# Optimization experiments

Measured on AMD Instinct MI355X. Metric: run time of the kernel, lower is better.

## Reference

```python
import jax, jax.numpy as jnp
import numpy as np

NQ = 7
D = 2 ** NQ              # 128
B = 1024
T = D * (D + 1) // 2     # 8256
DS = 0.25                # downscaling

_rows, _cols = np.tril_indices(D)
ROWS = jnp.asarray(_rows)
COLS = jnp.asarray(_cols)

_s = np.float32(1.0 / np.sqrt(2.0))
_H = np.array([[_s, _s], [_s, -_s]], dtype=np.complex64)          # Hadamard (X basis)
_Sdag = np.array([[1, 0], [0, -1j]], dtype=np.complex64)
GATES = jnp.asarray(np.stack([_H, _H @ _Sdag, np.eye(2)]).astype(np.complex64))  # [X, Y, Z] rotations, (3,2,2)


def _loss(flat, t, state_ri, tgt, basis):
    # Reconstruct real symmetric matrix from lower-triangular flatten: (B, D, D)
    M = (jnp.zeros((B, D, D), flat.dtype)
         .at[:, ROWS, COLS].set(flat)
         .at[:, COLS, ROWS].set(flat))
    # U = expm(-1j*DS*t*M); M is real symmetric so use eigh (exact, batched)
    w, V = jnp.linalg.eigh(M)                      # w:(B,D) V:(B,D,D)
    ang = DS * t[:, None] * w                      # (B, D)
    phase = (jnp.cos(ang) - 1j * jnp.sin(ang)).astype(jnp.complex64)
    Vc = V.astype(jnp.complex64)
    U = jnp.einsum('bik,bk,bjk->bij', Vc, phase, Vc)
    # Evolve initial state: U rho U^dagger
    rho0 = (state_ri[..., 0] + 1j * state_ri[..., 1]).astype(jnp.complex64)
    ev = U @ rho0 @ U.conj().swapaxes(-1, -2)
    # Per-sample Kronecker rotation: kron of per-qubit 2x2 gates (batched)
    rot = GATES[basis]                             # (B, NQ, 2, 2)
    full = rot[:, 0]
    for q in range(1, NQ):
        d = full.shape[-1]
        full = jnp.einsum('bij,bkl->bikjl', full, rot[:, q]).reshape(B, d * 2, d * 2)
    rr = full @ ev @ full.conj().swapaxes(-1, -2)
    # Measurement probabilities and NLL
    diag = jnp.diagonal(rr, axis1=-2, axis2=-1)    # (B, D)
    probs = jnp.abs(diag) ** 2
    probs = probs / probs.sum(axis=1, keepdims=True)
    tp = jnp.take_along_axis(probs, tgt[:, None], axis=1)[:, 0]
    tp = jnp.clip(tp, 1e-12, None)
    return -jnp.mean(jnp.log(tp)) / NQ


def setup_inputs() -> dict:
    key = jax.random.key(0)
    k1, k2, k3, k4, k5 = jax.random.split(key, 5)
    return {
        'predictor_flat': jax.random.normal(k1, (B, T), dtype=jnp.float32),
        'time': jax.random.uniform(k2, (B,), dtype=jnp.float32),
        'input_state': jax.random.normal(k3, (B, D, D, 2), dtype=jnp.float32),
        'target_indices': jax.random.randint(k4, (B,), 0, D),
        'basis_indices': jax.random.randint(k5, (B, NQ), 0, 3),
    }


def reference(predictor_flat, time, input_state, target_indices, basis_indices):
    return _loss(predictor_flat, time, input_state, target_indices, basis_indices)
```

## Files before the change

### kernel.cpp

```cpp
#include <hip/hip_runtime.h>
#include <math.h>

#define DD    128
#define NQQ   7
#define NB    1024
#define TRI   8256
#define NSQ   2
#define CSTR  136
#define FSTR  132

typedef short  bf16x8 __attribute__((ext_vector_type(8)));
typedef short  s16x4  __attribute__((ext_vector_type(4)));
typedef float  f32x16 __attribute__((ext_vector_type(16)));

__device__ __forceinline__ void split2(float v, unsigned short& h, unsigned short& l) {
  unsigned u = __builtin_bit_cast(unsigned, v);
  float hf = __builtin_bit_cast(float, u & 0xFFFF0000u);
  float lf = v - hf;
  h = (unsigned short)(u >> 16);
  l = (unsigned short)(__builtin_bit_cast(unsigned, lf) >> 16);
}
__device__ __forceinline__ float bf2f(unsigned short s) {
  return __builtin_bit_cast(float, ((unsigned)s) << 16);
}
__device__ __forceinline__ f32x16 MF(bf16x8 a, bf16x8 b, f32x16 c) {
  return __builtin_amdgcn_mfma_f32_32x32x16_bf16(a, b, c, 0, 0, 0);
}
__device__ __forceinline__ bf16x8 NEG(bf16x8 a) {
  int4 u = __builtin_bit_cast(int4, a);
  u.x ^= 0x80008000; u.y ^= 0x80008000; u.z ^= 0x80008000; u.w ^= 0x80008000;
  return __builtin_bit_cast(bf16x8, u);
}
__device__ __forceinline__ bf16x8 LDF(const unsigned short* C, int row, int s, int hb) {
  return *reinterpret_cast<const bf16x8*>(C + row * CSTR + s * 16 + hb * 8);
}

__global__ __launch_bounds__(512) __attribute__((amdgpu_waves_per_eu(2, 2)))
void loss_k(
    const float* __restrict__ flat,
    const float* __restrict__ timev,
    const float* __restrict__ state,
    const int*   __restrict__ tgt,
    const int*   __restrict__ basis,
    float* __restrict__ ws)
{
  __shared__ __align__(16) char lds[4 * 128 * CSTR * 2 + 8192];
  unsigned short* C0 = (unsigned short*)lds;
  unsigned short* C1 = C0 + 128 * CSTR;
  unsigned short* C2 = C1 + 128 * CSTR;
  unsigned short* C3 = C2 + 128 * CSTR;
  float* AUX = (float*)(lds + 4 * 128 * CSTR * 2);
  float* Urf = (float*)lds;
  float* Uif = Urf + 128 * FSTR;

  const int b    = blockIdx.x;
  const int tid  = threadIdx.x;
  const int wid  = tid >> 6;
  const int lane = tid & 63;
  const int l31  = lane & 31;
  const int hb   = lane >> 5;

  const int tr    = wid >> 1;
  const int tcb   = (wid & 1) * 2;
  const int arow  = 32 * tr + l31;
  const int bcol0 = 32 * tcb + l31;
  const int bcol1 = 32 * (tcb + 1) + l31;

  const float tval  = timev[b];
  const float alpha = 0.25f * tval * 0.25f;
  const float* fb = flat + (size_t)b * TRI;

#define STORE_TILE(PREG, SCALE, BCOL, DH, DL) do {                         \
    _Pragma("unroll")                                                      \
    for (int q_ = 0; q_ < 4; ++q_) {                                       \
      s16x4 hh_, ll_;                                                      \
      _Pragma("unroll")                                                    \
      for (int rr_ = 0; rr_ < 4; ++rr_) {                                  \
        unsigned short h_, l_;                                             \
        split2((SCALE) * (PREG)[4 * q_ + rr_], h_, l_);                    \
        hh_[rr_] = (short)h_; ll_[rr_] = (short)l_;                        \
      }                                                                    \
      int off_ = (BCOL) * CSTR + 32 * tr + 8 * q_ + 4 * hb;                \
      *(s16x4*)((DH) + off_) = hh_; *(s16x4*)((DL) + off_) = ll_;          \
    }                                                                      \
  } while (0)

  for (int e = tid; e < DD * DD; e += 512) {
    int i = e >> 7, j = e & 127;
    int r = i >= j ? i : j, c = i >= j ? j : i;
    float v = alpha * fb[(r * (r + 1)) / 2 + c];
    unsigned short h, l; split2(v, h, l);
    C0[i * CSTR + j] = h;  C1[i * CSTR + j] = l;
  }
  __syncthreads();

  f32x16 p0, p1, Cc0, Cc1, Qc0, Qc1;

#pragma unroll
  for (int e = 0; e < 16; ++e) { p0[e] = 0.0f; p1[e] = 0.0f; }
#pragma unroll
  for (int s = 0; s < 8; ++s) {
    bf16x8 ah = LDF(C0, arow, s, hb),  al = LDF(C1, arow, s, hb);
    bf16x8 b0h = LDF(C0, bcol0, s, hb), b0l = LDF(C1, bcol0, s, hb);
    bf16x8 b1h = LDF(C0, bcol1, s, hb), b1l = LDF(C1, bcol1, s, hb);
    p0 = MF(ah, b0h, p0); p0 = MF(ah, b0l, p0); p0 = MF(al, b0h, p0);
    p1 = MF(ah, b1h, p1); p1 = MF(ah, b1l, p1); p1 = MF(al, b1h, p1);
  }
  __syncthreads();
#pragma unroll
  for (int q = 0; q < 4; ++q) {
#pragma unroll
    for (int rr = 0; rr < 4; ++rr) {
      int e = 4 * q + rr;
      int rg = 32 * tr + 8 * q + 4 * hb + rr;
      float i0 = (rg == bcol0) ? 1.0f : 0.0f;
      float i1 = (rg == bcol1) ? 1.0f : 0.0f;
      Cc0[e] = i0 - 0.5f * p0[e];            Cc1[e] = i1 - 0.5f * p1[e];
      Qc0[e] = i0 - 0.16666667f * p0[e];     Qc1[e] = i1 - 0.16666667f * p1[e];
    }
  }
  STORE_TILE(p0, 1.0f, bcol0, C2, C3);
  STORE_TILE(p1, 1.0f, bcol1, C2, C3);
  __syncthreads();

#pragma unroll
  for (int e = 0; e < 16; ++e) { p0[e] = 0.0f; p1[e] = 0.0f; }
#pragma unroll
  for (int s = 0; s < 8; ++s) {
    bf16x8 ah = LDF(C2, arow, s, hb),  al = LDF(C3, arow, s, hb);
    bf16x8 b0h = LDF(C2, bcol0, s, hb), b0l = LDF(C3, bcol0, s, hb);
    bf16x8 b1h = LDF(C2, bcol1, s, hb), b1l = LDF(C3, bcol1, s, hb);
    p0 = MF(ah, b0h, p0); p0 = MF(ah, b0l, p0); p0 = MF(al, b0h, p0);
    p1 = MF(ah, b1h, p1); p1 = MF(ah, b1l, p1); p1 = MF(al, b1h, p1);
  }
  __syncthreads();
#pragma unroll
  for (int e = 0; e < 16; ++e) {
    Cc0[e] += 4.1666668e-2f * p0[e];  Cc1[e] += 4.1666668e-2f * p1[e];
    Qc0[e] += 8.3333333e-3f * p0[e];  Qc1[e] += 8.3333333e-3f * p1[e];
  }
  STORE_TILE(p0, 1.0f, bcol0, C0, C1);
  STORE_TILE(p1, 1.0f, bcol1, C0, C1);
  __syncthreads();

  const float CJ[9] = {0.f, 0.f, 0.f, -1.3888889e-3f, 2.4801587e-5f,
                       -2.7557319e-7f, 2.0876757e-9f, -1.1470746e-11f, 4.7794773e-14f};
  const float QJ[8] = {0.f, 0.f, 0.f, -1.9841270e-4f, 2.7557319e-6f,
                       -2.5052108e-8f, 1.6059044e-10f, -7.6471637e-13f};
#pragma unroll
  for (int j = 3; j <= 8; ++j) {
#pragma unroll
    for (int e = 0; e < 16; ++e) { p0[e] = 0.0f; p1[e] = 0.0f; }
#pragma unroll
    for (int s = 0; s < 8; ++s) {
      bf16x8 ah = LDF(C2, arow, s, hb),  al = LDF(C3, arow, s, hb);
      bf16x8 b0h = LDF(C0, bcol0, s, hb), b0l = LDF(C1, bcol0, s, hb);
      bf16x8 b1h = LDF(C0, bcol1, s, hb), b1l = LDF(C1, bcol1, s, hb);
      p0 = MF(ah, b0h, p0); p0 = MF(ah, b0l, p0); p0 = MF(al, b0h, p0);
      p1 = MF(ah, b1h, p1); p1 = MF(ah, b1l, p1); p1 = MF(al, b1h, p1);
    }
    __syncthreads();
#pragma unroll
    for (int e = 0; e < 16; ++e) { Cc0[e] += CJ[j] * p0[e]; Cc1[e] += CJ[j] * p1[e]; }
    if (j < 8) {
#pragma unroll
      for (int e = 0; e < 16; ++e) { Qc0[e] += QJ[j] * p0[e]; Qc1[e] += QJ[j] * p1[e]; }
      STORE_TILE(p0, 1.0f, bcol0, C0, C1);
      STORE_TILE(p1, 1.0f, bcol1, C0, C1);
    }
    __syncthreads();
  }

  STORE_TILE(Qc0, 1.0f, bcol0, C2, C3);
  STORE_TILE(Qc1, 1.0f, bcol1, C2, C3);
  for (int e = tid; e < DD * DD; e += 512) {
    int i = e >> 7, j = e & 127;
    int r = i >= j ? i : j, c = i >= j ? j : i;
    float v = alpha * fb[(r * (r + 1)) / 2 + c];
    unsigned short h, l; split2(v, h, l);
    C0[i * CSTR + j] = h;  C1[i * CSTR + j] = l;
  }
  __syncthreads();

#pragma unroll
  for (int e = 0; e < 16; ++e) { p0[e] = 0.0f; p1[e] = 0.0f; }
#pragma unroll
  for (int s = 0; s < 8; ++s) {
    bf16x8 ah = LDF(C0, arow, s, hb),  al = LDF(C1, arow, s, hb);
    bf16x8 b0h = LDF(C2, bcol0, s, hb), b0l = LDF(C3, bcol0, s, hb);
    bf16x8 b1h = LDF(C2, bcol1, s, hb), b1l = LDF(C3, bcol1, s, hb);
    p0 = MF(ah, b0h, p0); p0 = MF(ah, b0l, p0); p0 = MF(al, b0h, p0);
    p1 = MF(ah, b1h, p1); p1 = MF(ah, b1l, p1); p1 = MF(al, b1h, p1);
  }
  __syncthreads();

  STORE_TILE(Cc0, 1.0f, bcol0, C0, C1);
  STORE_TILE(Cc1, 1.0f, bcol1, C0, C1);
  STORE_TILE(p0, -1.0f, bcol0, C2, C3);
  STORE_TILE(p1, -1.0f, bcol1, C2, C3);
  __syncthreads();

  for (int sq = 0; sq < NSQ; ++sq) {
    f32x16 cr0, ci0, cr1, ci1;
#pragma unroll
    for (int e = 0; e < 16; ++e) { cr0[e] = 0; ci0[e] = 0; cr1[e] = 0; ci1[e] = 0; }
#pragma unroll
    for (int s = 0; s < 8; ++s) {
      bf16x8 aRh = LDF(C0, arow, s, hb), aRl = LDF(C1, arow, s, hb);
      bf16x8 aIh = LDF(C2, arow, s, hb), aIl = LDF(C3, arow, s, hb);
      bf16x8 aIhN = NEG(aIh), aIlN = NEG(aIl);
      bf16x8 bRh0 = LDF(C0, bcol0, s, hb), bRl0 = LDF(C1, bcol0, s, hb);
      bf16x8 bIh0 = LDF(C2, bcol0, s, hb), bIl0 = LDF(C3, bcol0, s, hb);
      bf16x8 bRh1 = LDF(C0, bcol1, s, hb), bRl1 = LDF(C1, bcol1, s, hb);
      bf16x8 bIh1 = LDF(C2, bcol1, s, hb), bIl1 = LDF(C3, bcol1, s, hb);
      cr0 = MF(aRh, bRh0, cr0); cr0 = MF(aRh, bRl0, cr0); cr0 = MF(aRl, bRh0, cr0);
      cr0 = MF(aIhN, bIh0, cr0); cr0 = MF(aIhN, bIl0, cr0); cr0 = MF(aIlN, bIh0, cr0);
      ci0 = MF(aRh, bIh0, ci0); ci0 = MF(aRh, bIl0, ci0); ci0 = MF(aRl, bIh0, ci0);
      cr1 = MF(aRh, bRh1, cr1); cr1 = MF(aRh, bRl1, cr1); cr1 = MF(aRl, bRh1, cr1);
      cr1 = MF(aIhN, bIh1, cr1); cr1 = MF(aIhN, bIl1, cr1); cr1 = MF(aIlN, bIh1, cr1);
      ci1 = MF(aRh, bIh1, ci1); ci1 = MF(aRh, bIl1, ci1); ci1 = MF(aRl, bIh1, ci1);
    }
    __syncthreads();
    if (sq < NSQ - 1) {
      STORE_TILE(cr0, 1.0f, bcol0, C0, C1);
      STORE_TILE(ci0, 2.0f, bcol0, C2, C3);
      STORE_TILE(cr1, 1.0f, bcol1, C0, C1);
      STORE_TILE(ci1, 2.0f, bcol1, C2, C3);
    } else {
#pragma unroll
      for (int q = 0; q < 4; ++q) {
        int off0 = bcol0 * FSTR + 32 * tr + 8 * q + 4 * hb;
        int off1 = bcol1 * FSTR + 32 * tr + 8 * q + 4 * hb;
        *(float4*)(Urf + off0) = make_float4(cr0[4*q], cr0[4*q+1], cr0[4*q+2], cr0[4*q+3]);
        *(float4*)(Uif + off0) = make_float4(2.0f*ci0[4*q], 2.0f*ci0[4*q+1], 2.0f*ci0[4*q+2], 2.0f*ci0[4*q+3]);
        *(float4*)(Urf + off1) = make_float4(cr1[4*q], cr1[4*q+1], cr1[4*q+2], cr1[4*q+3]);
        *(float4*)(Uif + off1) = make_float4(2.0f*ci1[4*q], 2.0f*ci1[4*q+1], 2.0f*ci1[4*q+2], 2.0f*ci1[4*q+3]);
      }
    }
    __syncthreads();
  }

  const int* bq = basis + b * NQQ;
  const float sv = 0.70710678118654752f;
  for (int q = 0; q < NQQ; ++q) {
    int g = bq[q];
    if (g == 2) continue;
    const int bit = 6 - q;
    float g00r, g01r, g01i, g10r, g11r, g11i;
    if (g == 0) { g00r = sv; g01r = sv; g01i = 0;   g10r = sv; g11r = -sv; g11i = 0;  }
    else        { g00r = sv; g01r = 0;  g01i = -sv; g10r = sv; g11r = 0;   g11i = sv; }
    for (int jj = tid; jj < 64 * 32; jj += 512) {
      int cg = jj & 31;
      int p  = jj >> 5;
      int low = p & ((1 << bit) - 1);
      int i0 = ((p >> bit) << (bit + 1)) | low;
      int i1 = i0 | (1 << bit);
      float4 a0 = *(float4*)(Urf + i0 * FSTR + 4 * cg);
      float4 b0 = *(float4*)(Uif + i0 * FSTR + 4 * cg);
      float4 a1 = *(float4*)(Urf + i1 * FSTR + 4 * cg);
      float4 b1 = *(float4*)(Uif + i1 * FSTR + 4 * cg);
      float4 n0r, n0i, n1r, n1i;
#define BFLY(cc) { \
      float A0 = a0.cc, B0 = b0.cc, A1 = a1.cc, B1 = b1.cc; \
      n0r.cc = g00r * A0 + g01r * A1 - g01i * B1; \
      n0i.cc = g00r * B0 + g01r * B1 + g01i * A1; \
      n1r.cc = g10r * A0 + g11r * A1 - g11i * B1; \
      n1i.cc = g10r * B0 + g11r * B1 + g11i * A1; }
      BFLY(x) BFLY(y) BFLY(z) BFLY(w)
#undef BFLY
      *(float4*)(Urf + i0 * FSTR + 4 * cg) = n0r;
      *(float4*)(Uif + i0 * FSTR + 4 * cg) = n0i;
      *(float4*)(Urf + i1 * FSTR + 4 * cg) = n1r;
      *(float4*)(Uif + i1 * FSTR + 4 * cg) = n1i;
    }
    __syncthreads();
  }

  {
    const int i  = tid >> 2;
    const int j0 = (tid & 3) * 32;
    float vr[32], vi[32];
#pragma unroll
    for (int c = 0; c < 8; ++c) {
      float4 x = *(float4*)(Urf + i * FSTR + j0 + 4 * c);
      vr[4*c+0] = x.x; vr[4*c+1] = x.y; vr[4*c+2] = x.z; vr[4*c+3] = x.w;
      float4 y = *(float4*)(Uif + i * FSTR + j0 + 4 * c);
      vi[4*c+0] = y.x; vi[4*c+1] = y.y; vi[4*c+2] = y.z; vi[4*c+3] = y.w;
    }
    __syncthreads();
#pragma unroll
    for (int blkc = 0; blkc < 4; ++blkc) {
      bf16x8 h, lo, h2, lo2;
#pragma unroll
      for (int e2 = 0; e2 < 8; ++e2) {
        unsigned short hh, ll;
        split2(vr[blkc * 8 + e2], hh, ll);  h[e2] = (short)hh;  lo[e2] = (short)ll;
        split2(vi[blkc * 8 + e2], hh, ll);  h2[e2] = (short)hh; lo2[e2] = (short)ll;
      }
      int off = i * CSTR + j0 + blkc * 8;
      *(bf16x8*)(C0 + off) = h;  *(bf16x8*)(C1 + off) = lo;
      *(bf16x8*)(C2 + off) = h2; *(bf16x8*)(C3 + off) = lo2;
    }
    __syncthreads();
  }

  const int slab = wid >> 1;
  const int part = wid & 1;
  const float* srow = state + (size_t)b * (DD * DD * 2) + (size_t)(32 * slab + l31) * 256;

#pragma unroll 1
  for (int ch = 0; ch < 2; ++ch) {
    const int n40 = 2 * ch;
    const int n41 = 2 * ch + 1;
    f32x16 w0, w1;
#pragma unroll
    for (int e = 0; e < 16; ++e) { w0[e] = 0; w1[e] = 0; }

    for (int s = 0; s < 8; ++s) {
      const float* pp = srow + (s * 16 + hb * 8) * 2;
      float4 q0 = *(const float4*)(pp);
      float4 q1 = *(const float4*)(pp + 4);
      float4 q2 = *(const float4*)(pp + 8);
      float4 q3 = *(const float4*)(pp + 12);
      float re[8] = {q0.x, q0.z, q1.x, q1.z, q2.x, q2.z, q3.x, q3.z};
      float im[8] = {q0.y, q0.w, q1.y, q1.w, q2.y, q2.w, q3.y, q3.w};
      bf16x8 rh, rl, ihh, ill;
#pragma unroll
      for (int e2 = 0; e2 < 8; ++e2) {
        unsigned short hh, ll;
        split2(re[e2], hh, ll); rh[e2] = (short)hh;  rl[e2] = (short)ll;
        split2(im[e2], hh, ll); ihh[e2] = (short)hh; ill[e2] = (short)ll;
      }
      bf16x8 rhn = NEG(rh), rln = NEG(rl);
#define P4N4(WREG, N4) do {                                                \
    int gcol_ = 32 * (N4) + l31;                                           \
    bf16x8 gRh = LDF(C0, gcol_, s, hb), gRl = LDF(C1, gcol_, s, hb);       \
    bf16x8 gIh = LDF(C2, gcol_, s, hb), gIl = LDF(C3, gcol_, s, hb);       \
    if (part == 0) {                                                       \
      WREG = MF(rh, gRh, WREG);  WREG = MF(rh, gRl, WREG);  WREG = MF(rl, gRh, WREG); \
      WREG = MF(ihh, gIh, WREG); WREG = MF(ihh, gIl, WREG); WREG = MF(ill, gIh, WREG); \
    } else {                                                               \
      WREG = MF(ihh, gRh, WREG); WREG = MF(ihh, gRl, WREG); WREG = MF(ill, gRh, WREG); \
      WREG = MF(rhn, gIh, WREG); WREG = MF(rhn, gIl, WREG); WREG = MF(rln, gIh, WREG); \
    }                                                                      \
  } while (0)
      P4N4(w0, n40); P4N4(w1, n41);
#undef P4N4
    }

#define P4DOT(WREG, N4) do {                                               \
    int gcol_ = 32 * (N4) + l31;                                           \
    float a1 = 0.0f, a2 = 0.0f;                                            \
    _Pragma("unroll")                                                      \
    for (int q_ = 0; q_ < 4; ++q_) {                                       \
      int koff = 32 * slab + 8 * q_ + 4 * hb;                              \
      s16x4 grh = *(const s16x4*)(C0 + gcol_ * CSTR + koff);               \
      s16x4 grl = *(const s16x4*)(C1 + gcol_ * CSTR + koff);               \
      s16x4 gih = *(const s16x4*)(C2 + gcol_ * CSTR + koff);               \
      s16x4 gil = *(const s16x4*)(C3 + gcol_ * CSTR + koff);               \
      _Pragma("unroll")                                                    \
      for (int rr_ = 0; rr_ < 4; ++rr_) {                                  \
        float wv = WREG[4 * q_ + rr_];                                     \
        float gr = bf2f((unsigned short)grh[rr_]) + bf2f((unsigned short)grl[rr_]); \
        float gi = bf2f((unsigned short)gih[rr_]) + bf2f((unsigned short)gil[rr_]); \
        a1 = fmaf(gr, wv, a1); a2 = fmaf(gi, wv, a2);                      \
      }                                                                    \
    }                                                                      \
    a1 += __shfl_xor(a1, 32); a2 += __shfl_xor(a2, 32);                    \
    if (lane < 32) {                                                       \
      AUX[((part * 2 + 0) * 4 + slab) * 128 + 32 * (N4) + l31] = a1;       \
      AUX[((part * 2 + 1) * 4 + slab) * 128 + 32 * (N4) + l31] = a2;       \
    }                                                                      \
  } while (0)
    P4DOT(w0, n40); P4DOT(w1, n41);
#undef P4DOT
  }
  __syncthreads();

  if (tid < 128) {
    float s0 = 0, s1 = 0, s2 = 0, s3 = 0;
#pragma unroll
    for (int sl = 0; sl < 4; ++sl) {
      s0 += AUX[(0 * 4 + sl) * 128 + tid];
      s1 += AUX[(1 * 4 + sl) * 128 + tid];
      s2 += AUX[(2 * 4 + sl) * 128 + tid];
      s3 += AUX[(3 * 4 + sl) * 128 + tid];
    }
    float dr = s0 - s3, di = s2 + s1;
    AUX[tid] = dr * dr + di * di;
  }
  __syncthreads();
  if (tid < 64) {
    float ps = AUX[tid] + AUX[tid + 64];
#pragma unroll
    for (int o = 32; o >= 1; o >>= 1) ps += __shfl_xor(ps, o);
    if (tid == 0) {
      float pt = AUX[tgt[b]];
      float tp = fmaxf(pt / ps, 1e-12f);
      ws[b] = -logf(tp) * (1.0f / (float)NQQ);
    }
  }
#undef STORE_TILE
}

__global__ __launch_bounds__(256) void reduce_k(const float* __restrict__ ws,
                                                float* __restrict__ out)
{
  __shared__ float s[256];
  const int tid = threadIdx.x;
  float v = ws[tid] + ws[tid + 256] + ws[tid + 512] + ws[tid + 768];
  s[tid] = v;
  __syncthreads();
  for (int o = 128; o > 0; o >>= 1) {
    if (tid < o) s[tid] += s[tid + o];
    __syncthreads();
  }
  if (tid == 0) out[0] = s[0] * (1.0f / (float)NB);
}

extern "C" void kernel_launch(void* const* d_in, const int* in_sizes, int n_in,
                              void* d_out, int out_size, void* d_ws, size_t ws_size,
                              hipStream_t stream) {
  const float* flat  = (const float*)d_in[0];
  const float* tv    = (const float*)d_in[1];
  const float* st    = (const float*)d_in[2];
  const int*   tgt   = (const int*)d_in[3];
  const int*   basis = (const int*)d_in[4];
  float* out = (float*)d_out;
  float* ws  = (float*)d_ws;

  hipLaunchKernelGGL(loss_k, dim3(NB), dim3(512), 0, stream,
                     flat, tv, st, tgt, basis, ws);
  hipLaunchKernelGGL(reduce_k, dim3(1), dim3(256), 0, stream, ws, out);
}
```

Baseline: 523.0 us.

## Double block to 1024 threads with one output tile per wave and bf16-split butterflies

Grows the block from 512 to 1024 threads, so each of the 16 waves computes a single 32x32 MFMA tile instead of two, and the final state-product loop runs as one pass with the work spread across more waves. The Kronecker butterfly stage now operates directly on the split bf16 hi/lo LDS buffers instead of a separate fp32 copy of U. This removes the fp32 staging pass and its conversion back to bf16. In exchange, register budget per thread drops, the waves_per_eu hint is removed, and every butterfly pass pays extra split and recombine arithmetic.

Result: slower. 935.9 us (+78.9%).

```diff
diff --git a/kernel.cpp b/kernel.cpp
--- a/kernel.cpp
+++ b/kernel.cpp
@@ -5,9 +5,7 @@
 #define NQQ   7
 #define NB    1024
 #define TRI   8256
-#define NSQ   2
 #define CSTR  136
-#define FSTR  132
 
 typedef short  bf16x8 __attribute__((ext_vector_type(8)));
 typedef short  s16x4  __attribute__((ext_vector_type(4)));
@@ -35,8 +33,7 @@
   return *reinterpret_cast<const bf16x8*>(C + row * CSTR + s * 16 + hb * 8);
 }
 
-__global__ __launch_bounds__(512) __attribute__((amdgpu_waves_per_eu(2, 2)))
-void loss_k(
+__global__ __launch_bounds__(1024) void loss_k(
     const float* __restrict__ flat,
     const float* __restrict__ timev,
     const float* __restrict__ state,
@@ -50,8 +47,6 @@
   unsigned short* C2 = C1 + 128 * CSTR;
   unsigned short* C3 = C2 + 128 * CSTR;
   float* AUX = (float*)(lds + 4 * 128 * CSTR * 2);
-  float* Urf = (float*)lds;
-  float* Uif = Urf + 128 * FSTR;
 
   const int b    = blockIdx.x;
   const int tid  = threadIdx.x;
@@ -60,17 +55,16 @@
   const int l31  = lane & 31;
   const int hb   = lane >> 5;
 
-  const int tr    = wid >> 1;
-  const int tcb   = (wid & 1) * 2;
-  const int arow  = 32 * tr + l31;
-  const int bcol0 = 32 * tcb + l31;
-  const int bcol1 = 32 * (tcb + 1) + l31;
+  const int tr   = wid >> 2;
+  const int tc   = wid & 3;
+  const int arow = 32 * tr + l31;
+  const int bcol = 32 * tc + l31;
 
   const float tval  = timev[b];
   const float alpha = 0.25f * tval * 0.25f;
   const float* fb = flat + (size_t)b * TRI;
 
-#define STORE_TILE(PREG, SCALE, BCOL, DH, DL) do {                         \
+#define STORE_TILE(PREG, SCALE, DH, DL) do {                               \
     _Pragma("unroll")                                                      \
     for (int q_ = 0; q_ < 4; ++q_) {                                       \
       s16x4 hh_, ll_;                                                      \
@@ -80,12 +74,23 @@
         split2((SCALE) * (PREG)[4 * q_ + rr_], h_, l_);                    \
         hh_[rr_] = (short)h_; ll_[rr_] = (short)l_;                        \
       }                                                                    \
-      int off_ = (BCOL) * CSTR + 32 * tr + 8 * q_ + 4 * hb;                \
+      int off_ = bcol * CSTR + 32 * tr + 8 * q_ + 4 * hb;                  \
       *(s16x4*)((DH) + off_) = hh_; *(s16x4*)((DL) + off_) = ll_;          \
     }                                                                      \
   } while (0)
 
-  for (int e = tid; e < DD * DD; e += 512) {
+#define PROD(AH, AL, BH, BL) do {                                          \
+    _Pragma("unroll")                                                      \
+    for (int e_ = 0; e_ < 16; ++e_) p[e_] = 0.0f;                          \
+    _Pragma("unroll")                                                      \
+    for (int s_ = 0; s_ < 8; ++s_) {                                       \
+      bf16x8 ah_ = LDF(AH, arow, s_, hb), al_ = LDF(AL, arow, s_, hb);     \
+      bf16x8 bh_ = LDF(BH, bcol, s_, hb), bl_ = LDF(BL, bcol, s_, hb);     \
+      p = MF(ah_, bh_, p); p = MF(ah_, bl_, p); p = MF(al_, bh_, p);       \
+    }                                                                      \
+  } while (0)
+
+  for (int e = tid; e < DD * DD; e += 1024) {
     int i = e >> 7, j = e & 127;
     int r = i >= j ? i : j, c = i >= j ? j : i;
     float v = alpha * fb[(r * (r + 1)) / 2 + c];
@@ -94,86 +99,56 @@
   }
   __syncthreads();
 
-  f32x16 p0, p1, Cc0, Cc1, Qc0, Qc1;
-
-#pragma unroll
-  for (int e = 0; e < 16; ++e) { p0[e] = 0.0f; p1[e] = 0.0f; }
-#pragma unroll
-  for (int s = 0; s < 8; ++s) {
-    bf16x8 ah = LDF(C0, arow, s, hb),  al = LDF(C1, arow, s, hb);
-    bf16x8 b0h = LDF(C0, bcol0, s, hb), b0l = LDF(C1, bcol0, s, hb);
-    bf16x8 b1h = LDF(C0, bcol1, s, hb), b1l = LDF(C1, bcol1, s, hb);
-    p0 = MF(ah, b0h, p0); p0 = MF(ah, b0l, p0); p0 = MF(al, b0h, p0);
-    p1 = MF(ah, b1h, p1); p1 = MF(ah, b1l, p1); p1 = MF(al, b1h, p1);
-  }
+  f32x16 p, Cc, Qc;
+
+  PROD(C0, C1, C0, C1);
   __syncthreads();
 #pragma unroll
   for (int q = 0; q < 4; ++q) {
 #pragma unroll
     for (int rr = 0; rr < 4; ++rr) {
       int e = 4 * q + rr;
-      int rg = 32 * tr + 8 * q + 4 * hb + rr;
-      float i0 = (rg == bcol0) ? 1.0f : 0.0f;
-      float i1 = (rg == bcol1) ? 1.0f : 0.0f;
-      Cc0[e] = i0 - 0.5f * p0[e];            Cc1[e] = i1 - 0.5f * p1[e];
-      Qc0[e] = i0 - 0.16666667f * p0[e];     Qc1[e] = i1 - 0.16666667f * p1[e];
-    }
-  }
-  STORE_TILE(p0, 1.0f, bcol0, C2, C3);
-  STORE_TILE(p1, 1.0f, bcol1, C2, C3);
-  __syncthreads();
-
-#pragma unroll
-  for (int e = 0; e < 16; ++e) { p0[e] = 0.0f; p1[e] = 0.0f; }
-#pragma unroll
-  for (int s = 0; s < 8; ++s) {
-    bf16x8 ah = LDF(C2, arow, s, hb),  al = LDF(C3, arow, s, hb);
-    bf16x8 b0h = LDF(C2, bcol0, s, hb), b0l = LDF(C3, bcol0, s, hb);
-    bf16x8 b1h = LDF(C2, bcol1, s, hb), b1l = LDF(C3, bcol1, s, hb);
-    p0 = MF(ah, b0h, p0); p0 = MF(ah, b0l, p0); p0 = MF(al, b0h, p0);
-    p1 = MF(ah, b1h, p1); p1 = MF(ah, b1l, p1); p1 = MF(al, b1h, p1);
-  }
+      float i0 = ((32 * tr + 8 * q + 4 * hb + rr) == bcol) ? 1.0f : 0.0f;
+      Cc[e] = i0 - 0.5f * p[e];
+      Qc[e] = i0 - 0.16666667f * p[e];
+    }
+  }
+  STORE_TILE(p, 1.0f, C2, C3);
+  __syncthreads();
+
+  PROD(C2, C3, C2, C3);
   __syncthreads();
 #pragma unroll
   for (int e = 0; e < 16; ++e) {
-    Cc0[e] += 4.1666668e-2f * p0[e];  Cc1[e] += 4.1666668e-2f * p1[e];
-    Qc0[e] += 8.3333333e-3f * p0[e];  Qc1[e] += 8.3333333e-3f * p1[e];
-  }
-  STORE_TILE(p0, 1.0f, bcol0, C0, C1);
-  STORE_TILE(p1, 1.0f, bcol1, C0, C1);
-  __syncthreads();
-
-  const float CJ[9] = {0.f, 0.f, 0.f, -1.3888889e-3f, 2.4801587e-5f,
-                       -2.7557319e-7f, 2.0876757e-9f, -1.1470746e-11f, 4.7794773e-14f};
-  const float QJ[8] = {0.f, 0.f, 0.f, -1.9841270e-4f, 2.7557319e-6f,
-                       -2.5052108e-8f, 1.6059044e-10f, -7.6471637e-13f};
-#pragma unroll
-  for (int j = 3; j <= 8; ++j) {
-#pragma unroll
-    for (int e = 0; e < 16; ++e) { p0[e] = 0.0f; p1[e] = 0.0f; }
-#pragma unroll
-    for (int s = 0; s < 8; ++s) {
-      bf16x8 ah = LDF(C2, arow, s, hb),  al = LDF(C3, arow, s, hb);
-      bf16x8 b0h = LDF(C0, bcol0, s, hb), b0l = LDF(C1, bcol0, s, hb);
-      bf16x8 b1h = LDF(C0, bcol1, s, hb), b1l = LDF(C1, bcol1, s, hb);
-      p0 = MF(ah, b0h, p0); p0 = MF(ah, b0l, p0); p0 = MF(al, b0h, p0);
-      p1 = MF(ah, b1h, p1); p1 = MF(ah, b1l, p1); p1 = MF(al, b1h, p1);
-    }
-    __syncthreads();
-#pragma unroll
-    for (int e = 0; e < 16; ++e) { Cc0[e] += CJ[j] * p0[e]; Cc1[e] += CJ[j] * p1[e]; }
-    if (j < 8) {
-#pragma unroll
-      for (int e = 0; e < 16; ++e) { Qc0[e] += QJ[j] * p0[e]; Qc1[e] += QJ[j] * p1[e]; }
-      STORE_TILE(p0, 1.0f, bcol0, C0, C1);
-      STORE_TILE(p1, 1.0f, bcol1, C0, C1);
-    }
-    __syncthreads();
-  }
-
-  STORE_TILE(Qc0, 1.0f, bcol0, C2, C3);
-  STORE_TILE(Qc1, 1.0f, bcol1, C2, C3);
-  for (int e = tid; e < DD * DD; e += 512) {
+    Cc[e] += 4.1666668e-2f * p[e];
+    Qc[e] += 8.3333333e-3f * p[e];
+  }
+  STORE_TILE(p, 1.0f, C0, C1);
+  __syncthreads();
+
+#define JSTEP(CJLIT, QJLIT, DO_STORE) do {                                 \
+    PROD(C2, C3, C0, C1);                                                  \
+    __syncthreads();                                                       \
+    _Pragma("unroll")                                                      \
+    for (int e_ = 0; e_ < 16; ++e_) Cc[e_] += (CJLIT) * p[e_];             \
+    if (DO_STORE) {                                                        \
+      _Pragma("unroll")                                                    \
+      for (int e_ = 0; e_ < 16; ++e_) Qc[e_] += (QJLIT) * p[e_];           \
+      STORE_TILE(p, 1.0f, C0, C1);                                         \
+    }                                                                      \
+    __syncthreads();                                                       \
+  } while (0)
+
+  JSTEP(-1.3888889e-3f,  -1.9841270e-4f,  1);
+  JSTEP( 2.4801587e-5f,   2.7557319e-6f,  1);
+  JSTEP(-2.7557319e-7f,  -2.5052108e-8f,  1);
+  JSTEP( 2.0876757e-9f,   1.6059044e-10f, 1);
+  JSTEP(-1.1470746e-11f, -7.6471637e-13f, 1);
+  JSTEP( 4.7794773e-14f,  0.0f,           0);
+#undef JSTEP
+
+  STORE_TILE(Qc, 1.0f, C2, C3);
+  for (int e = tid; e < DD * DD; e += 1024) {
     int i = e >> 7, j = e & 127;
     int r = i >= j ? i : j, c = i >= j ? j : i;
     float v = alpha * fb[(r * (r + 1)) / 2 + c];
@@ -182,61 +157,30 @@
   }
   __syncthreads();
 
-#pragma unroll
-  for (int e = 0; e < 16; ++e) { p0[e] = 0.0f; p1[e] = 0.0f; }
-#pragma unroll
-  for (int s = 0; s < 8; ++s) {
-    bf16x8 ah = LDF(C0, arow, s, hb),  al = LDF(C1, arow, s, hb);
-    bf16x8 b0h = LDF(C2, bcol0, s, hb), b0l = LDF(C3, bcol0, s, hb);
-    bf16x8 b1h = LDF(C2, bcol1, s, hb), b1l = LDF(C3, bcol1, s, hb);
-    p0 = MF(ah, b0h, p0); p0 = MF(ah, b0l, p0); p0 = MF(al, b0h, p0);
-    p1 = MF(ah, b1h, p1); p1 = MF(ah, b1l, p1); p1 = MF(al, b1h, p1);
-  }
-  __syncthreads();
-
-  STORE_TILE(Cc0, 1.0f, bcol0, C0, C1);
-  STORE_TILE(Cc1, 1.0f, bcol1, C0, C1);
-  STORE_TILE(p0, -1.0f, bcol0, C2, C3);
-  STORE_TILE(p1, -1.0f, bcol1, C2, C3);
-  __syncthreads();
-
-  for (int sq = 0; sq < NSQ; ++sq) {
-    f32x16 cr0, ci0, cr1, ci1;
-#pragma unroll
-    for (int e = 0; e < 16; ++e) { cr0[e] = 0; ci0[e] = 0; cr1[e] = 0; ci1[e] = 0; }
+  PROD(C0, C1, C2, C3);
+  __syncthreads();
+  STORE_TILE(Cc, 1.0f, C0, C1);
+  STORE_TILE(p, -1.0f, C2, C3);
+  __syncthreads();
+
+  for (int sq = 0; sq < 2; ++sq) {
+    f32x16 cr, ci;
+#pragma unroll
+    for (int e = 0; e < 16; ++e) { cr[e] = 0.0f; ci[e] = 0.0f; }
 #pragma unroll
     for (int s = 0; s < 8; ++s) {
       bf16x8 aRh = LDF(C0, arow, s, hb), aRl = LDF(C1, arow, s, hb);
       bf16x8 aIh = LDF(C2, arow, s, hb), aIl = LDF(C3, arow, s, hb);
-      bf16x8 aIhN = NEG(aIh), aIlN = NEG(aIl);
-      bf16x8 bRh0 = LDF(C0, bcol0, s, hb), bRl0 = LDF(C1, bcol0, s, hb);
-      bf16x8 bIh0 = LDF(C2, bcol0, s, hb), bIl0 = LDF(C3, bcol0, s, hb);
-      bf16x8 bRh1 = LDF(C0, bcol1, s, hb), bRl1 = LDF(C1, bcol1, s, hb);
-      bf16x8 bIh1 = LDF(C2, bcol1, s, hb), bIl1 = LDF(C3, bcol1, s, hb);
-      cr0 = MF(aRh, bRh0, cr0); cr0 = MF(aRh, bRl0, cr0); cr0 = MF(aRl, bRh0, cr0);
-      cr0 = MF(aIhN, bIh0, cr0); cr0 = MF(aIhN, bIl0, cr0); cr0 = MF(aIlN, bIh0, cr0);
-      ci0 = MF(aRh, bIh0, ci0); ci0 = MF(aRh, bIl0, ci0); ci0 = MF(aRl, bIh0, ci0);
-      cr1 = MF(aRh, bRh1, cr1); cr1 = MF(aRh, bRl1, cr1); cr1 = MF(aRl, bRh1, cr1);
-      cr1 = MF(aIhN, bIh1, cr1); cr1 = MF(aIhN, bIl1, cr1); cr1 = MF(aIlN, bIh1, cr1);
-      ci1 = MF(aRh, bIh1, ci1); ci1 = MF(aRh, bIl1, ci1); ci1 = MF(aRl, bIh1, ci1);
+      bf16x8 bRh = LDF(C0, bcol, s, hb), bRl = LDF(C1, bcol, s, hb);
+      bf16x8 bIh = LDF(C2, bcol, s, hb), bIl = LDF(C3, bcol, s, hb);
+      cr = MF(aRh, bRh, cr); cr = MF(aRh, bRl, cr); cr = MF(aRl, bRh, cr);
+      bf16x8 nIh = NEG(aIh), nIl = NEG(aIl);
+      cr = MF(nIh, bIh, cr); cr = MF(nIh, bIl, cr); cr = MF(nIl, bIh, cr);
+      ci = MF(aRh, bIh, ci); ci = MF(aRh, bIl, ci); ci = MF(aRl, bIh, ci);
     }
     __syncthreads();
-    if (sq < NSQ - 1) {
-      STORE_TILE(cr0, 1.0f, bcol0, C0, C1);
-      STORE_TILE(ci0, 2.0f, bcol0, C2, C3);
-      STORE_TILE(cr1, 1.0f, bcol1, C0, C1);
-      STORE_TILE(ci1, 2.0f, bcol1, C2, C3);
-    } else {
-#pragma unroll
-      for (int q = 0; q < 4; ++q) {
-        int off0 = bcol0 * FSTR + 32 * tr + 8 * q + 4 * hb;
-        int off1 = bcol1 * FSTR + 32 * tr + 8 * q + 4 * hb;
-        *(float4*)(Urf + off0) = make_float4(cr0[4*q], cr0[4*q+1], cr0[4*q+2], cr0[4*q+3]);
-        *(float4*)(Uif + off0) = make_float4(2.0f*ci0[4*q], 2.0f*ci0[4*q+1], 2.0f*ci0[4*q+2], 2.0f*ci0[4*q+3]);
-        *(float4*)(Urf + off1) = make_float4(cr1[4*q], cr1[4*q+1], cr1[4*q+2], cr1[4*q+3]);
-        *(float4*)(Uif + off1) = make_float4(2.0f*ci1[4*q], 2.0f*ci1[4*q+1], 2.0f*ci1[4*q+2], 2.0f*ci1[4*q+3]);
-      }
-    }
+    STORE_TILE(cr, 1.0f, C0, C1);
+    STORE_TILE(ci, 2.0f, C2, C3);
     __syncthreads();
   }
 
@@ -249,89 +193,81 @@
     float g00r, g01r, g01i, g10r, g11r, g11i;
     if (g == 0) { g00r = sv; g01r = sv; g01i = 0;   g10r = sv; g11r = -sv; g11i = 0;  }
     else        { g00r = sv; g01r = 0;  g01i = -sv; g10r = sv; g11r = 0;   g11i = sv; }
-    for (int jj = tid; jj < 64 * 32; jj += 512) {
+#pragma unroll 1
+    for (int jj = tid; jj < 64 * 32; jj += 1024) {
       int cg = jj & 31;
-      int p  = jj >> 5;
-      int low = p & ((1 << bit) - 1);
-      int i0 = ((p >> bit) << (bit + 1)) | low;
+      int pr = jj >> 5;
+      int low = pr & ((1 << bit) - 1);
+      int i0 = ((pr >> bit) << (bit + 1)) | low;
       int i1 = i0 | (1 << bit);
-      float4 a0 = *(float4*)(Urf + i0 * FSTR + 4 * cg);
-      float4 b0 = *(float4*)(Uif + i0 * FSTR + 4 * cg);
-      float4 a1 = *(float4*)(Urf + i1 * FSTR + 4 * cg);
-      float4 b1 = *(float4*)(Uif + i1 * FSTR + 4 * cg);
-      float4 n0r, n0i, n1r, n1i;
-#define BFLY(cc) { \
-      float A0 = a0.cc, B0 = b0.cc, A1 = a1.cc, B1 = b1.cc; \
-      n0r.cc = g00r * A0 + g01r * A1 - g01i * B1; \
-      n0i.cc = g00r * B0 + g01r * B1 + g01i * A1; \
-      n1r.cc = g10r * A0 + g11r * A1 - g11i * B1; \
-      n1i.cc = g10r * B0 + g11r * B1 + g11i * A1; }
-      BFLY(x) BFLY(y) BFLY(z) BFLY(w)
-#undef BFLY
-      *(float4*)(Urf + i0 * FSTR + 4 * cg) = n0r;
-      *(float4*)(Uif + i0 * FSTR + 4 * cg) = n0i;
-      *(float4*)(Urf + i1 * FSTR + 4 * cg) = n1r;
-      *(float4*)(Uif + i1 * FSTR + 4 * cg) = n1i;
+      int base0 = i0 * CSTR + 4 * cg;
+      int base1 = i1 * CSTR + 4 * cg;
+      s16x4 A0h = *(s16x4*)(C0 + base0), A0l = *(s16x4*)(C1 + base0);
+      s16x4 B0h = *(s16x4*)(C2 + base0), B0l = *(s16x4*)(C3 + base0);
+      s16x4 A1h = *(s16x4*)(C0 + base1), A1l = *(s16x4*)(C1 + base1);
+      s16x4 B1h = *(s16x4*)(C2 + base1), B1l = *(s16x4*)(C3 + base1);
+      s16x4 oA0h, oA0l, oB0h, oB0l, oA1h, oA1l, oB1h, oB1l;
+#pragma unroll
+      for (int d = 0; d < 4; ++d) {
+        float a0 = bf2f((unsigned short)A0h[d]) + bf2f((unsigned short)A0l[d]);
+        float b0 = bf2f((unsigned short)B0h[d]) + bf2f((unsigned short)B0l[d]);
+        float a1 = bf2f((unsigned short)A1h[d]) + bf2f((unsigned short)A1l[d]);
+        float b1 = bf2f((unsigned short)B1h[d]) + bf2f((unsigned short)B1l[d]);
+        float n0r = g00r * a0 + g01r * a1 - g01i * b1;
+        float n0i = g00r * b0 + g01r * b1 + g01i * a1;
+        float n1r = g10r * a0 + g11r * a1 - g11i * b1;
+        float n1i = g10r * b0 + g11r * b1 + g11i * a1;
+        unsigned short h, l;
+        split2(n0r, h, l); oA0h[d] = (short)h; oA0l[d] = (short)l;
+        split2(n0i, h, l); oB0h[d] = (short)h; oB0l[d] = (short)l;
+        split2(n1r, h, l); oA1h[d] = (short)h; oA1l[d] = (short)l;
+        split2(n1i, h, l); oB1h[d] = (short)h; oB1l[d] = (short)l;
+      }
+      *(s16x4*)(C0 + base0) = oA0h; *(s16x4*)(C1 + base0) = oA0l;
+      *(s16x4*)(C2 + base0) = oB0h; *(s16x4*)(C3 + base0) = oB0l;
+      *(s16x4*)(C0 + base1) = oA1h; *(s16x4*)(C1 + base1) = oA1l;
+      *(s16x4*)(C2 + base1) = oB1h; *(s16x4*)(C3 + base1) = oB1l;
     }
     __syncthreads();
   }
 
-  {
-    const int i  = tid >> 2;
-    const int j0 = (tid & 3) * 32;
-    float vr[32], vi[32];
-#pragma unroll
-    for (int c = 0; c < 8; ++c) {
-      float4 x = *(float4*)(Urf + i * FSTR + j0 + 4 * c);
-      vr[4*c+0] = x.x; vr[4*c+1] = x.y; vr[4*c+2] = x.z; vr[4*c+3] = x.w;
-      float4 y = *(float4*)(Uif + i * FSTR + j0 + 4 * c);
-      vi[4*c+0] = y.x; vi[4*c+1] = y.y; vi[4*c+2] = y.z; vi[4*c+3] = y.w;
-    }
-    __syncthreads();
-#pragma unroll
-    for (int blkc = 0; blkc < 4; ++blkc) {
-      bf16x8 h, lo, h2, lo2;
-#pragma unroll
-      for (int e2 = 0; e2 < 8; ++e2) {
-        unsigned short hh, ll;
-        split2(vr[blkc * 8 + e2], hh, ll);  h[e2] = (short)hh;  lo[e2] = (short)ll;
-        split2(vi[blkc * 8 + e2], hh, ll);  h2[e2] = (short)hh; lo2[e2] = (short)ll;
-      }
-      int off = i * CSTR + j0 + blkc * 8;
-      *(bf16x8*)(C0 + off) = h;  *(bf16x8*)(C1 + off) = lo;
-      *(bf16x8*)(C2 + off) = h2; *(bf16x8*)(C3 + off) = lo2;
-    }
-    __syncthreads();
-  }
-
-  const int slab = wid >> 1;
-  const int part = wid & 1;
+  const int part = wid >> 3;
+  const int slab = (wid >> 1) & 3;
+  const int n40  = (wid & 1) * 2;
+  const int n41  = n40 + 1;
   const float* srow = state + (size_t)b * (DD * DD * 2) + (size_t)(32 * slab + l31) * 256;
 
-#pragma unroll 1
-  for (int ch = 0; ch < 2; ++ch) {
-    const int n40 = 2 * ch;
-    const int n41 = 2 * ch + 1;
-    f32x16 w0, w1;
-#pragma unroll
-    for (int e = 0; e < 16; ++e) { w0[e] = 0; w1[e] = 0; }
-
-    for (int s = 0; s < 8; ++s) {
-      const float* pp = srow + (s * 16 + hb * 8) * 2;
-      float4 q0 = *(const float4*)(pp);
-      float4 q1 = *(const float4*)(pp + 4);
-      float4 q2 = *(const float4*)(pp + 8);
-      float4 q3 = *(const float4*)(pp + 12);
-      float re[8] = {q0.x, q0.z, q1.x, q1.z, q2.x, q2.z, q3.x, q3.z};
-      float im[8] = {q0.y, q0.w, q1.y, q1.w, q2.y, q2.w, q3.y, q3.w};
-      bf16x8 rh, rl, ihh, ill;
-#pragma unroll
-      for (int e2 = 0; e2 < 8; ++e2) {
-        unsigned short hh, ll;
-        split2(re[e2], hh, ll); rh[e2] = (short)hh;  rl[e2] = (short)ll;
-        split2(im[e2], hh, ll); ihh[e2] = (short)hh; ill[e2] = (short)ll;
-      }
-      bf16x8 rhn = NEG(rh), rln = NEG(rl);
+  f32x16 w0, w1;
+#pragma unroll
+  for (int e = 0; e < 16; ++e) { w0[e] = 0.0f; w1[e] = 0.0f; }
+
+  for (int s = 0; s < 8; ++s) {
+    const float* pp = srow + (s * 16 + hb * 8) * 2;
+    float4 q0 = *(const float4*)(pp);
+    float4 q1 = *(const float4*)(pp + 4);
+    float4 q2 = *(const float4*)(pp + 8);
+    float4 q3 = *(const float4*)(pp + 12);
+    bf16x8 rh, rl, ihh, ill;
+    {
+      unsigned short h, l;
+      split2(q0.x, h, l); rh[0] = (short)h; rl[0] = (short)l;
+      split2(q0.z, h, l); rh[1] = (short)h; rl[1] = (short)l;
+      split2(q1.x, h, l); rh[2] = (short)h; rl[2] = (short)l;
+      split2(q1.z, h, l); rh[3] = (short)h; rl[3] = (short)l;
+      split2(q2.x, h, l); rh[4] = (short)h; rl[4] = (short)l;
+      split2(q2.z, h, l); rh[5] = (short)h; rl[5] = (short)l;
+      split2(q3.x, h, l); rh[6] = (short)h; rl[6] = (short)l;
+      split2(q3.z, h, l); rh[7] = (short)h; rl[7] = (short)l;
+      split2(q0.y, h, l); ihh[0] = (short)h; ill[0] = (short)l;
+      split2(q0.w, h, l); ihh[1] = (short)h; ill[1] = (short)l;
+      split2(q1.y, h, l); ihh[2] = (short)h; ill[2] = (short)l;
+      split2(q1.w, h, l); ihh[3] = (short)h; ill[3] = (short)l;
+      split2(q2.y, h, l); ihh[4] = (short)h; ill[4] = (short)l;
+      split2(q2.w, h, l); ihh[5] = (short)h; ill[5] = (short)l;
+      split2(q3.y, h, l); ihh[6] = (short)h; ill[6] = (short)l;
+      split2(q3.w, h, l); ihh[7] = (short)h; ill[7] = (short)l;
+    }
+    bf16x8 rhn = NEG(rh), rln = NEG(rl);
 #define P4N4(WREG, N4) do {                                                \
     int gcol_ = 32 * (N4) + l31;                                           \
     bf16x8 gRh = LDF(C0, gcol_, s, hb), gRl = LDF(C1, gcol_, s, hb);       \
@@ -344,9 +280,9 @@
       WREG = MF(rhn, gIh, WREG); WREG = MF(rhn, gIl, WREG); WREG = MF(rln, gIh, WREG); \
     }                                                                      \
   } while (0)
-      P4N4(w0, n40); P4N4(w1, n41);
+    P4N4(w0, n40); P4N4(w1, n41);
 #undef P4N4
-    }
+  }
 
 #define P4DOT(WREG, N4) do {                                               \
     int gcol_ = 32 * (N4) + l31;                                           \
@@ -372,9 +308,8 @@
       AUX[((part * 2 + 1) * 4 + slab) * 128 + 32 * (N4) + l31] = a2;       \
     }                                                                      \
   } while (0)
-    P4DOT(w0, n40); P4DOT(w1, n41);
+  P4DOT(w0, n40); P4DOT(w1, n41);
 #undef P4DOT
-  }
   __syncthreads();
 
   if (tid < 128) {
@@ -401,6 +336,7 @@
     }
   }
 #undef STORE_TILE
+#undef PROD
 }
 
 __global__ __launch_bounds__(256) void reduce_k(const float* __restrict__ ws,
@@ -429,7 +365,7 @@
   float* out = (float*)d_out;
   float* ws  = (float*)d_ws;
 
-  hipLaunchKernelGGL(loss_k, dim3(NB), dim3(512), 0, stream,
+  hipLaunchKernelGGL(loss_k, dim3(NB), dim3(1024), 0, stream,
                      flat, tv, st, tgt, basis, ws);
   hipLaunchKernelGGL(reduce_k, dim3(1), dim3(256), 0, stream, ws, out);
 }
```
